# Kernel tuning notes

Measured on AMD Instinct MI355X. Metric: run time of the kernel, lower is better.

Reference implementation:

```python
import jax, jax.numpy as jnp
import numpy as np

N_C = 64
D = 128

def setup_inputs() -> dict:
    key = jax.random.key(0)
    embeddings = jax.random.normal(key, (1024, N_C * D), dtype=jnp.float32)
    return {"embeddings": embeddings}

def reference(embeddings) -> jnp.ndarray:
    two_b, _ = embeddings.shape
    B = two_b // 2
    # (2, B, n_c, d), softmax over last dim
    q = jax.nn.softmax(embeddings.reshape(2, B, N_C, D), axis=-1)
    q_a, q_b = q[0], q[1]  # (B, n_c, d)

    self_sim_loss = -(q_a * q_b).sum() / (B * N_C)

    q_a2 = q_a * q_a
    q_b2 = q_b * q_b
    # Faithful to the repeat/repeat_interleave + bmm: block (i, j) of the
    # (n_c^2, d, d) product equals q2[:, j].T @ q2[:, i]  -> einsum over batch.
    prod_a = jnp.einsum('bjc,bid->ijcd', q_a2, q_a2)  # (n_c, n_c, d, d)
    prod_b = jnp.einsum('bjc,bid->ijcd', q_b2, q_b2)

    # mask out diagonal cluster pairs i == j (done before sqrt in original;
    # entries are strictly positive so masking after sqrt is identical)
    offdiag = (~jnp.eye(N_C, dtype=bool))[:, :, None, None]  # (n_c, n_c, 1, 1)

    raw_a = jnp.where(offdiag, jnp.sqrt(prod_a), 0.0).sum()
    raw_b = jnp.where(offdiag, jnp.sqrt(prod_b), 0.0).sum()

    scale = (N_C * N_C - N_C) * (B ** 0.5)
    cluster_loss = -(raw_a / scale + raw_b / scale) / 2
    return self_sim_loss + cluster_loss
```

## Files before the change

### kernel.cpp

```cpp
#include <hip/hip_runtime.h>
#include <cstdint>
#include <cstddef>

#define NCLUS 64
#define DIM   128
#define BATCH 512
#define QCOLS 8192
#define NPAIR 2016
#define TSTRB (QCOLS * BATCH)
#define FP8SCALE 256.0f

typedef float f32x4 __attribute__((ext_vector_type(4)));
typedef long  lx2  __attribute__((ext_vector_type(2)));


__device__ __forceinline__ void ld_lds16(const void* g, void* l) {
  __builtin_amdgcn_global_load_lds(
      (__attribute__((address_space(1))) void*)g,
      (__attribute__((address_space(3))) void*)l, 16, 0, 0);
}

#define SYNC_VM4()  asm volatile("s_waitcnt vmcnt(4)\n\ts_barrier" ::: "memory")
#define SYNC_VM0()  asm volatile("s_waitcnt vmcnt(0)\n\ts_barrier" ::: "memory")
#define SYNC_LGKM() asm volatile("s_waitcnt lgkmcnt(0)\n\ts_barrier" ::: "memory")

__global__ __launch_bounds__(256) void softmax_q2_kernel(
    const float* __restrict__ emb, uint8_t* __restrict__ q2t,
    float* __restrict__ dotPart) {
  __shared__ uint32_t T32[2 * 64 * 33];
  __shared__ float red[4];
  const int c  = blockIdx.y;
  const int bq = blockIdx.x;
  const int tid = threadIdx.x;
  const int w = tid >> 6, lane = tid & 63;
  const int sub = lane >> 5;
  const int col = lane & 31;

  float4 qa = {0.f, 0.f, 0.f, 0.f};
  float dot = 0.f;

#pragma unroll
  for (int k = 0; k < 16; ++k) {
    const int t  = k & 1;
    const int bl = w * 16 + (k >> 1) * 2 + sub;
    const int b  = bq * 64 + bl;
    const float4 v = *(const float4*)(emb +
        ((size_t)(t * BATCH + b) * QCOLS + (size_t)c * DIM + col * 4));

    float mx = fmaxf(fmaxf(v.x, v.y), fmaxf(v.z, v.w));
#pragma unroll
    for (int off = 1; off < 32; off <<= 1) mx = fmaxf(mx, __shfl_xor(mx, off));
    float e0 = __expf(v.x - mx), e1 = __expf(v.y - mx);
    float e2 = __expf(v.z - mx), e3 = __expf(v.w - mx);
    float s = (e0 + e1) + (e2 + e3);
#pragma unroll
    for (int off = 1; off < 32; off <<= 1) s += __shfl_xor(s, off);
    const float inv = 1.0f / s;
    const float q0 = e0 * inv, q1 = e1 * inv, q2 = e2 * inv, q3 = e3 * inv;

    if (t == 0) { qa.x = q0; qa.y = q1; qa.z = q2; qa.w = q3; }
    else        { dot += qa.x * q0 + qa.y * q1 + qa.z * q2 + qa.w * q3; }

    int pk = __builtin_amdgcn_cvt_pk_fp8_f32(q0 * q0 * FP8SCALE,
                                             q1 * q1 * FP8SCALE, 0, false);
    pk = __builtin_amdgcn_cvt_pk_fp8_f32(q2 * q2 * FP8SCALE,
                                         q3 * q3 * FP8SCALE, pk, true);
    T32[(t * 64 + bl) * 33 + col] = (uint32_t)pk;
  }
  __syncthreads();

#pragma unroll
  for (int it = 0; it < 4; ++it) {
    int ch = it * 256 + tid;
    int t = ch >> 9, d = (ch >> 2) & 127, b16 = ch & 3;
    const int dq = d >> 2, sh = (d & 3) * 8;
    uint32_t w0 = 0, w1 = 0, w2 = 0, w3 = 0;
#pragma unroll
    for (int r = 0; r < 4; ++r) {
      w0 |= ((T32[(t * 64 + b16 * 8 + r) * 33 + dq] >> sh) & 0xFFu) << (8 * r);
      w1 |= ((T32[(t * 64 + b16 * 8 + 4 + r) * 33 + dq] >> sh) & 0xFFu) << (8 * r);
      w2 |= ((T32[(t * 64 + 32 + b16 * 8 + r) * 33 + dq] >> sh) & 0xFFu) << (8 * r);
      w3 |= ((T32[(t * 64 + 32 + b16 * 8 + 4 + r) * 33 + dq] >> sh) & 0xFFu) << (8 * r);
    }
    size_t off = (size_t)t * TSTRB + (size_t)(c * DIM + d) * BATCH +
                 (size_t)bq * 64 + b16 * 16;
    uint4 o; o.x = w0; o.y = w1; o.z = w2; o.w = w3;
    *(uint4*)(q2t + off) = o;
  }

#pragma unroll
  for (int off = 1; off < 64; off <<= 1) dot += __shfl_xor(dot, off);
  if (lane == 0) red[w] = dot;
  __syncthreads();
  if (tid == 0) dotPart[blockIdx.y * 8 + blockIdx.x] = red[0] + red[1] + red[2] + red[3];
}

__global__ __launch_bounds__(256, 4) void gram_sqrt_kernel(
    const uint8_t* __restrict__ q2t, float* __restrict__ Spart) {
  __shared__ uint8_t L[32768 + 16];

  int sidx = ((int)blockIdx.x & 7) * 252 + ((int)blockIdx.x >> 3);
  int q = sidx, gi = 0;
  while (q >= 64 * gi + 28) { q -= 64 * gi + 28; ++gi; }
  int I, J;
  if (q < 64 * gi) {
    int gj = q >> 6, r = q & 63;
    I = gi * 8 + (r >> 3);
    J = gj * 8 + (r & 7);
  } else {
    int dq = q - 64 * gi;
    int il = 1;
    while (il * (il + 1) / 2 <= dq) ++il;
    I = gi * 8 + il;
    J = gi * 8 + (dq - il * (il - 1) / 2);
  }

  const uint8_t* baseA = q2t + (size_t)J * (DIM * BATCH);
  const uint8_t* baseB = q2t + (size_t)I * (DIM * BATCH);

  const int tid  = threadIdx.x;
  const int lane = tid & 63, w = tid >> 6;
  const int wm = w & 1, wn = w >> 1;

  const int t0 = tid, t1 = 256 + tid;
  const int r0s = t0 >> 2, r1s = t1 >> 2;
  const int c0s = ((t0 & 3) - ((r0s >> 1) & 3)) & 3;
  const int c1s = ((t1 & 3) - ((r1s >> 1) & 3)) & 3;
  const size_t g0 = (size_t)r0s * BATCH + c0s * 16;
  const size_t g1 = (size_t)r1s * BATCH + c1s * 16;
  uint8_t* Lb = L;
  const int ldsw = w * 1024;

  const int l15 = lane & 15, qtr = lane >> 4;
  const int sig = ((qtr + (l15 >> 1)) & 3) * 16;
  const int ApO = wm * 4096 + l15 * 64 + sig;
  const int BpO = 8192 + wn * 4096 + l15 * 64 + sig;

  f32x4 acc[4][4];
#pragma unroll
  for (int i = 0; i < 4; ++i)
#pragma unroll
    for (int j = 0; j < 4; ++j) acc[i][j] = (f32x4){0.f, 0.f, 0.f, 0.f};

  float S0 = 0.f, S1 = 0.f;

  ld_lds16(baseA + g0, Lb + ldsw);
  ld_lds16(baseA + g1, Lb + 4096 + ldsw);
  ld_lds16(baseB + g0, Lb + 8192 + ldsw);
  ld_lds16(baseB + g1, Lb + 12288 + ldsw);

  for (int m = 0; m < 16; ++m) {
    if (m < 15) {
      const int mi = m + 1;
      const int bb = (mi & 1) << 14;
      const size_t ck = (size_t)(mi >> 3) * TSTRB + (size_t)(mi & 7) * 64;
      ld_lds16(baseA + ck + g0, Lb + bb + ldsw);
      ld_lds16(baseA + ck + g1, Lb + bb + 4096 + ldsw);
      ld_lds16(baseB + ck + g0, Lb + bb + 8192 + ldsw);
      ld_lds16(baseB + ck + g1, Lb + bb + 12288 + ldsw);
      SYNC_VM4();
    } else {
      SYNC_VM0();
    }

    const int be = (m & 1) << 14;
    lx2 a[4], b[4];
#pragma unroll
    for (int i = 0; i < 4; ++i) {
      a[i] = *(const lx2*)(Lb + be + ApO + i * 1024);
      b[i] = *(const lx2*)(Lb + be + BpO + i * 1024);
    }
#pragma unroll
    for (int i = 0; i < 4; ++i)
#pragma unroll
      for (int j = 0; j < 4; ++j)
        acc[i][j] = __builtin_amdgcn_mfma_f32_16x16x32_fp8_fp8(a[i].x, b[j].x, acc[i][j], 0, 0, 0);
#pragma unroll
    for (int i = 0; i < 4; ++i)
#pragma unroll
      for (int j = 0; j < 4; ++j)
        acc[i][j] = __builtin_amdgcn_mfma_f32_16x16x32_fp8_fp8(a[i].y, b[j].y, acc[i][j], 0, 0, 0);

    if (m == 7) {
#pragma unroll
      for (int i = 0; i < 4; ++i)
#pragma unroll
        for (int j = 0; j < 4; ++j) {
#pragma unroll
          for (int e = 0; e < 4; ++e) S0 += sqrtf(acc[i][j][e]);
          acc[i][j] = (f32x4){0.f, 0.f, 0.f, 0.f};
        }
    }

    SYNC_LGKM();
  }

#pragma unroll
  for (int i = 0; i < 4; ++i)
#pragma unroll
    for (int j = 0; j < 4; ++j)
#pragma unroll
      for (int e = 0; e < 4; ++e) S1 += sqrtf(acc[i][j][e]);

  float local = (S0 + S1) * (1.0f / 256.0f);
#pragma unroll
  for (int off = 1; off < 64; off <<= 1) local += __shfl_xor(local, off);
  float* fred = (float*)(L + 32768);
  if (lane == 0) fred[w] = local;
  __syncthreads();
  if (tid == 0) Spart[blockIdx.x] = fred[0] + fred[1] + fred[2] + fred[3];
}

__global__ __launch_bounds__(256) void finalize_kernel(
    const float* __restrict__ P, float* __restrict__ out) {
  __shared__ float rd[8];
  const int tid = threadIdx.x;
  float d = 0.f, s = 0.f;
  for (int i = tid; i < 512; i += 256) d += P[i];
  for (int i = tid; i < NPAIR; i += 256) s += P[512 + i];
#pragma unroll
  for (int off = 1; off < 64; off <<= 1) { d += __shfl_xor(d, off); s += __shfl_xor(s, off); }
  const int w = tid >> 6;
  if ((tid & 63) == 0) { rd[w] = d; rd[4 + w] = s; }
  __syncthreads();
  if (tid == 0) {
    float dt = rd[0] + rd[1] + rd[2] + rd[3];
    float st = rd[4] + rd[5] + rd[6] + rd[7];
    out[0] = -dt / 32768.0f - st / (4032.0f * 22.62741699796952f);
  }
}

extern "C" void kernel_launch(void* const* d_in, const int* in_sizes, int n_in,
                              void* d_out, int out_size, void* d_ws, size_t ws_size,
                              hipStream_t stream) {
  const float* emb = (const float*)d_in[0];
  float* out = (float*)d_out;
  float* P = (float*)d_ws;
  uint8_t* q2t = (uint8_t*)d_ws + 16384;

  softmax_q2_kernel<<<dim3(8, 64), 256, 0, stream>>>(emb, q2t, P);
  gram_sqrt_kernel<<<dim3(NPAIR), 256, 0, stream>>>(q2t, P + 512);
  finalize_kernel<<<1, 256, 0, stream>>>(P, out);
}
```

Measured before the change: 133.7 us.

## Load gram operands directly from global into registers, dropping LDS staging

The gram kernel no longer stages fp8 tiles through LDS with async global-to-LDS loads and barriers. Each wave now loads its MFMA operands straight from global memory into registers, software-pipelined one k-step ahead, and occupancy bounds drop from 4 to 3 blocks per SM. This removes LDS traffic and per-step barriers. The cost is that waves sharing a block now load overlapping A/B data redundantly through L1/L2 and register pressure rises.

```diff
diff --git a/kernel.cpp b/kernel.cpp
--- a/kernel.cpp
+++ b/kernel.cpp
@@ -13,16 +13,6 @@
 typedef float f32x4 __attribute__((ext_vector_type(4)));
 typedef long  lx2  __attribute__((ext_vector_type(2)));
 
-
-__device__ __forceinline__ void ld_lds16(const void* g, void* l) {
-  __builtin_amdgcn_global_load_lds(
-      (__attribute__((address_space(1))) void*)g,
-      (__attribute__((address_space(3))) void*)l, 16, 0, 0);
-}
-
-#define SYNC_VM4()  asm volatile("s_waitcnt vmcnt(4)\n\ts_barrier" ::: "memory")
-#define SYNC_VM0()  asm volatile("s_waitcnt vmcnt(0)\n\ts_barrier" ::: "memory")
-#define SYNC_LGKM() asm volatile("s_waitcnt lgkmcnt(0)\n\ts_barrier" ::: "memory")
 
 __global__ __launch_bounds__(256) void softmax_q2_kernel(
     const float* __restrict__ emb, uint8_t* __restrict__ q2t,
@@ -95,9 +85,9 @@
   if (tid == 0) dotPart[blockIdx.y * 8 + blockIdx.x] = red[0] + red[1] + red[2] + red[3];
 }
 
-__global__ __launch_bounds__(256, 4) void gram_sqrt_kernel(
+__global__ __launch_bounds__(256, 3) void gram_sqrt_kernel(
     const uint8_t* __restrict__ q2t, float* __restrict__ Spart) {
-  __shared__ uint8_t L[32768 + 16];
+  __shared__ float red[4];
 
   int sidx = ((int)blockIdx.x & 7) * 252 + ((int)blockIdx.x >> 3);
   int q = sidx, gi = 0;
@@ -115,26 +105,18 @@
     J = gi * 8 + (dq - il * (il - 1) / 2);
   }
 
-  const uint8_t* baseA = q2t + (size_t)J * (DIM * BATCH);
-  const uint8_t* baseB = q2t + (size_t)I * (DIM * BATCH);
-
   const int tid  = threadIdx.x;
   const int lane = tid & 63, w = tid >> 6;
   const int wm = w & 1, wn = w >> 1;
-
-  const int t0 = tid, t1 = 256 + tid;
-  const int r0s = t0 >> 2, r1s = t1 >> 2;
-  const int c0s = ((t0 & 3) - ((r0s >> 1) & 3)) & 3;
-  const int c1s = ((t1 & 3) - ((r1s >> 1) & 3)) & 3;
-  const size_t g0 = (size_t)r0s * BATCH + c0s * 16;
-  const size_t g1 = (size_t)r1s * BATCH + c1s * 16;
-  uint8_t* Lb = L;
-  const int ldsw = w * 1024;
-
   const int l15 = lane & 15, qtr = lane >> 4;
-  const int sig = ((qtr + (l15 >> 1)) & 3) * 16;
-  const int ApO = wm * 4096 + l15 * 64 + sig;
-  const int BpO = 8192 + wn * 4096 + l15 * 64 + sig;
+
+  const uint8_t* Ab[4];
+  const uint8_t* Bb[4];
+#pragma unroll
+  for (int i = 0; i < 4; ++i) {
+    Ab[i] = q2t + (size_t)(J * DIM + wm * 64 + i * 16 + l15) * BATCH + qtr * 16;
+    Bb[i] = q2t + (size_t)(I * DIM + wn * 64 + i * 16 + l15) * BATCH + qtr * 16;
+  }
 
   f32x4 acc[4][4];
 #pragma unroll
@@ -144,44 +126,40 @@
 
   float S0 = 0.f, S1 = 0.f;
 
-  ld_lds16(baseA + g0, Lb + ldsw);
-  ld_lds16(baseA + g1, Lb + 4096 + ldsw);
-  ld_lds16(baseB + g0, Lb + 8192 + ldsw);
-  ld_lds16(baseB + g1, Lb + 12288 + ldsw);
-
-  for (int m = 0; m < 16; ++m) {
-    if (m < 15) {
-      const int mi = m + 1;
-      const int bb = (mi & 1) << 14;
-      const size_t ck = (size_t)(mi >> 3) * TSTRB + (size_t)(mi & 7) * 64;
-      ld_lds16(baseA + ck + g0, Lb + bb + ldsw);
-      ld_lds16(baseA + ck + g1, Lb + bb + 4096 + ldsw);
-      ld_lds16(baseB + ck + g0, Lb + bb + 8192 + ldsw);
-      ld_lds16(baseB + ck + g1, Lb + bb + 12288 + ldsw);
-      SYNC_VM4();
-    } else {
-      SYNC_VM0();
-    }
-
-    const int be = (m & 1) << 14;
-    lx2 a[4], b[4];
-#pragma unroll
-    for (int i = 0; i < 4; ++i) {
-      a[i] = *(const lx2*)(Lb + be + ApO + i * 1024);
-      b[i] = *(const lx2*)(Lb + be + BpO + i * 1024);
-    }
+  lx2 Ac[4], Bc[4];
+#pragma unroll
+  for (int i = 0; i < 4; ++i) {
+    Ac[i] = *(const lx2*)(Ab[i]);
+    Bc[i] = *(const lx2*)(Bb[i]);
+  }
+
+#pragma unroll
+  for (int tm = 0; tm < 16; ++tm) {
+    lx2 An[4], Bn[4];
+    if (tm < 15) {
+      const size_t noff = (size_t)((tm + 1) >> 3) * TSTRB +
+                          (size_t)((tm + 1) & 7) * 64;
+#pragma unroll
+      for (int i = 0; i < 4; ++i) {
+        An[i] = *(const lx2*)(Ab[i] + noff);
+        Bn[i] = *(const lx2*)(Bb[i] + noff);
+      }
+    }
+
 #pragma unroll
     for (int i = 0; i < 4; ++i)
 #pragma unroll
       for (int j = 0; j < 4; ++j)
-        acc[i][j] = __builtin_amdgcn_mfma_f32_16x16x32_fp8_fp8(a[i].x, b[j].x, acc[i][j], 0, 0, 0);
+        acc[i][j] = __builtin_amdgcn_mfma_f32_16x16x32_fp8_fp8(
+            Ac[i].x, Bc[j].x, acc[i][j], 0, 0, 0);
 #pragma unroll
     for (int i = 0; i < 4; ++i)
 #pragma unroll
       for (int j = 0; j < 4; ++j)
-        acc[i][j] = __builtin_amdgcn_mfma_f32_16x16x32_fp8_fp8(a[i].y, b[j].y, acc[i][j], 0, 0, 0);
-
-    if (m == 7) {
+        acc[i][j] = __builtin_amdgcn_mfma_f32_16x16x32_fp8_fp8(
+            Ac[i].y, Bc[j].y, acc[i][j], 0, 0, 0);
+
+    if (tm == 7) {
 #pragma unroll
       for (int i = 0; i < 4; ++i)
 #pragma unroll
@@ -192,7 +170,10 @@
         }
     }
 
-    SYNC_LGKM();
+    if (tm < 15) {
+#pragma unroll
+      for (int i = 0; i < 4; ++i) { Ac[i] = An[i]; Bc[i] = Bn[i]; }
+    }
   }
 
 #pragma unroll
@@ -205,10 +186,9 @@
   float local = (S0 + S1) * (1.0f / 256.0f);
 #pragma unroll
   for (int off = 1; off < 64; off <<= 1) local += __shfl_xor(local, off);
-  float* fred = (float*)(L + 32768);
-  if (lane == 0) fred[w] = local;
-  __syncthreads();
-  if (tid == 0) Spart[blockIdx.x] = fred[0] + fred[1] + fred[2] + fred[3];
+  if (lane == 0) red[w] = local;
+  __syncthreads();
+  if (tid == 0) Spart[blockIdx.x] = red[0] + red[1] + red[2] + red[3];
 }
 
 __global__ __launch_bounds__(256) void finalize_kernel(
```

Result: slower. 197.6 us (+47.8%).
